# Kernel tuning notes

Hardware: AMD Instinct MI355X
Metric: run time of the kernel (lower is better)

The kernel has to match this reference:

```python
import jax, jax.numpy as jnp
import numpy as np

B, S, H = 8, 512, 1024          # batch, seq_len, hidden_size
T, K, FF = 8, 2, 4096           # num_thoughts, top_k, ffn dim (4*H)
NH = 8                          # combiner attention heads
HD = H // NH
CREATIVITY = 1.0


def setup_inputs() -> dict:
    key = jax.random.key(0)
    ks = jax.random.split(key, 16)
    s = 0.02
    return {
        "hidden_states": jax.random.normal(ks[0], (B, S, H), jnp.float32),
        # router
        "router_w": jax.random.normal(ks[1], (H, T), jnp.float32) * s,
        "router_b": jnp.zeros((T,), jnp.float32),
        # thought branch FFNs (one per thought)
        "W1": jax.random.normal(ks[2], (T, H, FF), jnp.float32) * s,
        "b1": jnp.zeros((T, FF), jnp.float32),
        "W2": jax.random.normal(ks[3], (T, FF, H), jnp.float32) * s,
        "b2": jnp.zeros((T, H), jnp.float32),
        # attention combiner (MultiheadAttention proj weights)
        "Wq": jax.random.normal(ks[4], (H, H), jnp.float32) * s,
        "bq": jnp.zeros((H,), jnp.float32),
        "Wk": jax.random.normal(ks[5], (H, H), jnp.float32) * s,
        "bk": jnp.zeros((H,), jnp.float32),
        "Wv": jax.random.normal(ks[6], (H, H), jnp.float32) * s,
        "bv": jnp.zeros((H,), jnp.float32),
        "Wo": jax.random.normal(ks[7], (H, H), jnp.float32) * s,
        "bo": jnp.zeros((H,), jnp.float32),
    }


def reference(hidden_states, router_w, router_b, W1, b1, W2, b2,
              Wq, bq, Wk, bk, Wv, bv, Wo, bo):
    # ---- router: mean-pool -> linear -> softmax -> top-k ----
    pooled = hidden_states.mean(axis=1)                       # [B,H]
    router_probs = jax.nn.softmax(pooled @ router_w + router_b, axis=-1)  # [B,T]
    top_p, top_i = jax.lax.top_k(router_probs, K)             # [B,K]
    weights = jax.nn.softmax(top_p, axis=-1)                  # renormalized active weights [B,K]

    # ---- grouped branch FFN (gather expert weights, batched GEMMs) ----
    h = jnp.einsum('bsh,bkhf->bksf', hidden_states, W1[top_i]) + b1[top_i][:, :, None, :]
    h = jax.nn.gelu(h, approximate=False)
    branch_out = jnp.einsum('bksf,bkfh->bksh', h, W2[top_i]) + b2[top_i][:, :, None, :]
    branch_out = branch_out * CREATIVITY                      # [B,K,S,H]

    # ---- attention combiner over flattened thoughts [B, K*S, H] ----
    L = K * S
    flat = branch_out.reshape(B, L, H)
    q = (flat @ Wq + bq).reshape(B, L, NH, HD)
    k = (flat @ Wk + bk).reshape(B, L, NH, HD)
    v = (flat @ Wv + bv).reshape(B, L, NH, HD)
    scores = jnp.einsum('blhd,bmhd->bhlm', q, k) / jnp.sqrt(jnp.float32(HD))
    attn = jax.nn.softmax(scores, axis=-1)
    ctx = jnp.einsum('bhlm,bmhd->blhd', attn, v).reshape(B, L, H)
    attended = (ctx @ Wo + bo).reshape(B, K, S, H)

    combined = jnp.einsum('bksh,bk->bsh', attended, weights)  # [B,S,H]

    # ---- metrics ----
    entropy = jnp.mean(-jnp.sum(router_probs * jnp.log(router_probs + 1e-8), axis=1))
    a = branch_out[:, 0].reshape(B, -1)
    b_ = branch_out[:, 1].reshape(B, -1)
    cos = jnp.sum(a * b_, -1) / jnp.maximum(
        jnp.linalg.norm(a, axis=-1) * jnp.linalg.norm(b_, axis=-1), 1e-8)
    diversity = jnp.mean(1.0 - cos)
    return combined, entropy, diversity
```

## Files before the change

### kernel.cpp

```cpp
#include <hip/hip_runtime.h>
#include <hip/hip_bf16.h>
#include <math.h>

typedef float f32x4 __attribute__((ext_vector_type(4)));
typedef short s16x8 __attribute__((ext_vector_type(8)));
typedef short s16x4 __attribute__((ext_vector_type(4)));
typedef unsigned int u32;

#define DEVI __device__ __forceinline__

#define Bn   8
#define Sn   512
#define Hn   1024
#define Tn   8
#define Kn   2
#define FFn  4096
#define NHn  8
#define HDn  128
#define Ln   1024
#define OUT_COMBINED 4194304

DEVI unsigned short f2bf(float x) {
  __hip_bfloat16 h = __float2bfloat16(x);
  union { __hip_bfloat16 h; unsigned short u; } cv; cv.h = h; return cv.u;
}
DEVI float bf2f(unsigned short u) {
  union { u32 i; float f; } cv; cv.i = ((u32)u) << 16; return cv.f;
}

typedef __attribute__((address_space(3))) u32 lds_u32;
typedef __attribute__((address_space(1))) u32 glb_u32;
DEVI void gload16(const void* g, void* l) {
  __builtin_amdgcn_global_load_lds((const glb_u32*)g, (lds_u32*)l, 16, 0, 0);
}

__global__ __launch_bounds__(256) void pool_part_k(const float* __restrict__ hid, float* __restrict__ part)
{
  const int b = blockIdx.x, scn = blockIdx.y;
  const int hh = threadIdx.x * 4;
  float4 acc = make_float4(0.f, 0.f, 0.f, 0.f);
  const float* base = hid + ((long)b * Sn + (long)scn * 128) * Hn + hh;
  for (int s = 0; s < 128; ++s) {
    float4 v = *(const float4*)(base + (long)s * Hn);
    acc.x += v.x; acc.y += v.y; acc.z += v.z; acc.w += v.w;
  }
  *(float4*)(part + ((long)(scn * Bn + b)) * Hn + hh) = acc;
}

__global__ __launch_bounds__(256) void pool_final_k(const float* __restrict__ part, float* __restrict__ pooled)
{
  const int i = blockIdx.x * 256 + threadIdx.x;
  float s = 0.f;
  for (int sc = 0; sc < 4; ++sc) s += part[sc * (Bn * Hn) + i];
  pooled[i] = s * (1.f / (float)Sn);
}

__global__ __launch_bounds__(64) void router_k(
    const float* __restrict__ pooled, const float* __restrict__ rw, const float* __restrict__ rb,
    float* __restrict__ probs, int* __restrict__ topi, float* __restrict__ wts,
    int* __restrict__ flags, float* __restrict__ entropy_out)
{
  __shared__ float lg[64];
  __shared__ int sfl[8];
  __shared__ float sent[8];
  const int tid = threadIdx.x;
  const int b = tid >> 3, t = tid & 7;
  if (tid < 8) sfl[tid] = 0;
  float acc = rb[t];
  const float* pb = pooled + b * Hn;
  for (int i = 0; i < Hn; ++i) acc += pb[i] * rw[i * Tn + t];
  lg[tid] = acc;
  __syncthreads();
  if (t == 0) {
    float p[8];
    float mx = lg[b * 8];
    for (int i = 1; i < 8; ++i) mx = fmaxf(mx, lg[b * 8 + i]);
    float ssum = 0.f;
    for (int i = 0; i < 8; ++i) { p[i] = expf(lg[b * 8 + i] - mx); ssum += p[i]; }
    float ent = 0.f;
    for (int i = 0; i < 8; ++i) { p[i] /= ssum; ent -= p[i] * logf(p[i] + 1e-8f); probs[b * 8 + i] = p[i]; }
    sent[b] = ent;
    int i1 = 0;
    for (int i = 1; i < 8; ++i) if (p[i] > p[i1]) i1 = i;
    int i2 = (i1 == 0) ? 1 : 0;
    for (int i = 0; i < 8; ++i) if (i != i1 && p[i] > p[i2]) i2 = i;
    float w0 = 1.f / (1.f + expf(p[i2] - p[i1]));
    float w1 = 1.f / (1.f + expf(p[i1] - p[i2]));
    topi[b * 2] = i1; topi[b * 2 + 1] = i2;
    wts[b * 2] = w0; wts[b * 2 + 1] = w1;
    atomicOr(&sfl[i1], 1); atomicOr(&sfl[i2], 1);
  }
  __syncthreads();
  if (tid < 8) flags[tid] = sfl[tid];
  if (tid == 0) {
    float e = 0.f;
    for (int i = 0; i < 8; ++i) e += sent[i];
    entropy_out[0] = e * (1.f / (float)Bn);
  }
}

__global__ __launch_bounds__(256) void cvt_k(const float* __restrict__ in, unsigned short* __restrict__ out)
{
  const long i = ((long)blockIdx.x * 256 + threadIdx.x) * 4;
  float4 v = *(const float4*)(in + i);
  s16x4 o;
  o[0] = (short)f2bf(v.x); o[1] = (short)f2bf(v.y); o[2] = (short)f2bf(v.z); o[3] = (short)f2bf(v.w);
  *(s16x4*)(out + i) = o;
}

__global__ __launch_bounds__(256) void bias3_k(const float* __restrict__ bq, const float* __restrict__ bk,
                                               const float* __restrict__ bv, float* __restrict__ o)
{
  const int i = blockIdx.x * 256 + threadIdx.x;
  o[i] = bq[i]; o[i + 1024] = bk[i]; o[i + 2048] = bv[i];
}

__global__ __launch_bounds__(256) void transpose_k(const float* __restrict__ Win, unsigned short* __restrict__ Wout,
                                                   int Kd, int N, long sIn, long sOut, const int* __restrict__ flags)
{
  const int t = blockIdx.z;
  if (flags && flags[t] == 0) return;
  __shared__ float tile[64][65];
  const float* in = Win + (long)t * sIn;
  unsigned short* out = Wout + (long)t * sOut;
  const int kb = blockIdx.y * 64, nb = blockIdx.x * 64;
  const int tx = threadIdx.x & 15, ty = threadIdx.x >> 4;
  #pragma unroll
  for (int i = 0; i < 4; ++i) {
    const int r = ty + i * 16;
    float4 v = *(const float4*)(in + (long)(kb + r) * N + nb + tx * 4);
    tile[r][tx * 4 + 0] = v.x; tile[r][tx * 4 + 1] = v.y;
    tile[r][tx * 4 + 2] = v.z; tile[r][tx * 4 + 3] = v.w;
  }
  __syncthreads();
  #pragma unroll
  for (int i = 0; i < 4; ++i) {
    const int n = ty + i * 16;
    s16x4 o;
    #pragma unroll
    for (int j = 0; j < 4; ++j) o[j] = (short)f2bf(tile[tx * 4 + j][n]);
    *(s16x4*)(out + (long)(nb + n) * Kd + kb + tx * 4) = o;
  }
}

template<int EPI, int OUTMODE>
__global__ __launch_bounds__(256) void gemm_k(
    const unsigned short* __restrict__ A0, const unsigned short* __restrict__ Bt0,
    const float* __restrict__ bias0, unsigned short* __restrict__ C0,
    int N, int Kd,
    const int* __restrict__ topi, int kTop,
    long sA_b, long sA_p, long sBt_t, int sBias_t, long sC_p)
{
  __shared__ __align__(16) char smem[36864];
  const int z = blockIdx.z;
  const int bidx = kTop ? (z / kTop) : 0;
  const int t = topi ? topi[z] : 0;
  const unsigned short* A = A0 + (long)bidx * sA_b + (long)z * sA_p;
  const unsigned short* Bt = Bt0 + (long)t * sBt_t;
  const float* bias = bias0 + (long)t * sBias_t;
  unsigned short* C = C0 + (long)z * sC_p;

  const int m0 = blockIdx.y * 128;
  const int n0 = blockIdx.x * 128;
  const int tid = threadIdx.x;
  const int lane = tid & 63, w = tid >> 6;
  const int wm = w >> 1, wn = w & 1;

  const int srow = w * 32 + (lane >> 2);
  const int csw = ((lane & 3) ^ ((srow ^ (srow >> 2)) & 3)) << 4;

  const char* gA0 = (const char*)(A + (long)(m0 + srow) * Kd) + csw;
  const char* gA1 = (const char*)(A + (long)(m0 + srow + 16) * Kd) + csw;
  const char* gB0 = (const char*)(Bt + (long)(n0 + srow) * Kd) + csw;
  const char* gB1 = (const char*)(Bt + (long)(n0 + srow + 16) * Kd) + csw;

  char* ldsAw = smem + w * 2048;
  char* ldsBw = smem + 16384 + w * 2048;

  f32x4 acc[4][4];
  const f32x4 zero = {0.f, 0.f, 0.f, 0.f};
  #pragma unroll
  for (int i = 0; i < 4; ++i)
    #pragma unroll
    for (int j = 0; j < 4; ++j) acc[i][j] = zero;

  const int rA = lane & 15;
  const int cb = (lane >> 4) << 4;
  int aoff[4], boff[4];
  #pragma unroll
  for (int mi = 0; mi < 4; ++mi) {
    int row = wm * 64 + mi * 16 + rA;
    aoff[mi] = row * 64 + (cb ^ (((row ^ (row >> 2)) & 3) << 4));
    int rowb = wn * 64 + mi * 16 + rA;
    boff[mi] = rowb * 64 + (cb ^ (((rowb ^ (rowb >> 2)) & 3) << 4));
  }

  const int nIter = Kd >> 5;
  gload16(gA0, ldsAw);
  gload16(gA1, ldsAw + 1024);
  gload16(gB0, ldsBw);
  gload16(gB1, ldsBw + 1024);
  __syncthreads();

  int cur = 0;
  for (int it = 0; it < nIter; ++it) {
    if (it + 1 < nIter) {
      const long kb2 = (long)(it + 1) * 64;
      const int nb = cur ^ 1;
      gload16(gA0 + kb2, ldsAw + nb * 8192);
      gload16(gA1 + kb2, ldsAw + nb * 8192 + 1024);
      gload16(gB0 + kb2, ldsBw + nb * 8192);
      gload16(gB1 + kb2, ldsBw + nb * 8192 + 1024);
    }
    const char* pa = smem + cur * 8192;
    const char* pb = smem + 16384 + cur * 8192;
    s16x8 af[4], bfr[4];
    #pragma unroll
    for (int mi = 0; mi < 4; ++mi) af[mi] = *(const s16x8*)(pa + aoff[mi]);
    #pragma unroll
    for (int nj = 0; nj < 4; ++nj) bfr[nj] = *(const s16x8*)(pb + boff[nj]);
    __builtin_amdgcn_s_setprio(1);
    #pragma unroll
    for (int mi = 0; mi < 4; ++mi)
      #pragma unroll
      for (int nj = 0; nj < 4; ++nj)
        acc[mi][nj] = __builtin_amdgcn_mfma_f32_16x16x32_bf16(af[mi], bfr[nj], acc[mi][nj], 0, 0, 0);
    __builtin_amdgcn_s_setprio(0);
    __syncthreads();
    cur ^= 1;
  }

  unsigned short* et = (unsigned short*)(smem + w * 9216);
  const int r4 = (lane >> 4) << 2;
  const int nbase = n0 + wn * 64;
  const int seg = nbase >> 10;
  #pragma unroll
  for (int nj = 0; nj < 4; ++nj) {
    const int n = nbase + nj * 16 + rA;
    const float bv = bias[n];
    #pragma unroll
    for (int mi = 0; mi < 4; ++mi) {
      #pragma unroll
      for (int j = 0; j < 4; ++j) {
        float x = acc[mi][nj][j] + bv;
        if (EPI == 1) x = 0.5f * x * (1.0f + erff(x * 0.70710678118654752f));
        const int mrl = mi * 16 + r4 + j;
        const int ncl = nj * 16 + rA;
        if (OUTMODE == 0 || seg < 2) et[mrl * 72 + ncl] = f2bf(x);
        else                         et[ncl * 72 + mrl] = f2bf(x);
      }
    }
  }
  const int erow = lane >> 3, echunk = lane & 7;
  if (OUTMODE == 0) {
    const long r0 = m0 + wm * 64;
    #pragma unroll
    for (int rr = 0; rr < 8; ++rr) {
      const int row = rr * 8 + erow;
      s16x8 v = *(const s16x8*)(et + row * 72 + echunk * 8);
      *(s16x8*)(C + (r0 + row) * N + nbase + echunk * 8) = v;
    }
  } else {
    const int nseg = nbase & 1023;
    if (seg < 2) {
      unsigned short* dst = C + (long)seg * 8388608;
      const long r0 = m0 + wm * 64;
      #pragma unroll
      for (int rr = 0; rr < 8; ++rr) {
        const int row = rr * 8 + erow;
        s16x8 v = *(const s16x8*)(et + row * 72 + echunk * 8);
        *(s16x8*)(dst + (r0 + row) * 1024 + nseg + echunk * 8) = v;
      }
    } else {
      unsigned short* vtp = C + 16777216;
      const int bb = m0 >> 10;
      const int ltok0 = (m0 & 1023) + wm * 64;
      #pragma unroll
      for (int rr = 0; rr < 8; ++rr) {
        const int nrow = rr * 8 + erow;
        s16x8 v = *(const s16x8*)(et + nrow * 72 + echunk * 8);
        *(s16x8*)(vtp + ((long)(bb * 1024 + nseg + nrow)) * 1024 + ltok0 + echunk * 8) = v;
      }
    }
  }
}

__global__ __launch_bounds__(256) void flash_k(
    const unsigned short* __restrict__ q, const unsigned short* __restrict__ k,
    const unsigned short* __restrict__ vt, unsigned short* __restrict__ ctx)
{
  __shared__ unsigned short Ks[64 * 128];
  __shared__ unsigned short Vs[128 * 64];
  __shared__ unsigned short Ps[4][16 * 72];
  const int qt = blockIdx.x, h = blockIdx.y, b = blockIdx.z;
  const int tid = threadIdx.x, lane = tid & 63, w = tid >> 6;
  const int q0 = qt * 64;
  const int rA = lane & 15;

  const int qrow = q0 + w * 16 + rA;
  const unsigned short* qp = q + ((long)(b * Ln + qrow)) * Hn + h * HDn + ((lane >> 4) * 8);
  s16x8 qf[4];
  #pragma unroll
  for (int kk = 0; kk < 4; ++kk) qf[kk] = *(const s16x8*)(qp + kk * 32);

  f32x4 o[8];
  const f32x4 zero = {0.f, 0.f, 0.f, 0.f};
  #pragma unroll
  for (int i = 0; i < 8; ++i) o[i] = zero;
  float mrun[4], lrun[4];
  #pragma unroll
  for (int j = 0; j < 4; ++j) { mrun[j] = -1e30f; lrun[j] = 0.f; }

  const float sc = 0.08838834764831845f * 1.4426950408889634f;

  const int krow0 = w * 16 + (lane >> 4);
  const int kc = lane & 15;
  const int vrow0 = w * 32 + (lane >> 3);
  const int vc = lane & 7;

  for (int kvt = 0; kvt < 16; ++kvt) {
    const int kv0 = kvt * 64;
    __syncthreads();
    #pragma unroll
    for (int qq = 0; qq < 4; ++qq) {
      const int rk = krow0 + qq * 4;
      gload16(k + ((long)(b * Ln + kv0 + rk)) * Hn + h * HDn + ((kc ^ (rk & 7)) * 8),
              (char*)Ks + w * 4096 + qq * 1024);
      const int rv = vrow0 + qq * 8;
      gload16(vt + ((long)(b * 1024 + h * HDn + rv)) * Ln + kv0 + ((vc ^ (rv & 7)) * 8),
              (char*)Vs + w * 4096 + qq * 1024);
    }
    __syncthreads();

    f32x4 sacc[4];
    #pragma unroll
    for (int nj = 0; nj < 4; ++nj) sacc[nj] = zero;
    #pragma unroll
    for (int kk = 0; kk < 4; ++kk) {
      #pragma unroll
      for (int nj = 0; nj < 4; ++nj) {
        const int row = nj * 16 + rA;
        const int byt = row * 256 + (((kk * 4 + (lane >> 4)) ^ (row & 7)) << 4);
        s16x8 kf = *(const s16x8*)((const char*)Ks + byt);
        sacc[nj] = __builtin_amdgcn_mfma_f32_16x16x32_bf16(qf[kk], kf, sacc[nj], 0, 0, 0);
      }
    }

    #pragma unroll
    for (int j = 0; j < 4; ++j) {
      float s0 = sacc[0][j] * sc, s1 = sacc[1][j] * sc, s2 = sacc[2][j] * sc, s3 = sacc[3][j] * sc;
      float tmax = fmaxf(fmaxf(s0, s1), fmaxf(s2, s3));
      #pragma unroll
      for (int mm = 1; mm < 16; mm <<= 1) tmax = fmaxf(tmax, __shfl_xor(tmax, mm, 64));
      const float mn = fmaxf(mrun[j], tmax);
      const float al = exp2f(mrun[j] - mn);
      mrun[j] = mn;
      float p0 = exp2f(s0 - mn), p1 = exp2f(s1 - mn), p2 = exp2f(s2 - mn), p3 = exp2f(s3 - mn);
      float ts = p0 + p1 + p2 + p3;
      #pragma unroll
      for (int mm = 1; mm < 16; mm <<= 1) ts += __shfl_xor(ts, mm, 64);
      lrun[j] = lrun[j] * al + ts;
      #pragma unroll
      for (int nn = 0; nn < 8; ++nn) o[nn][j] *= al;
      const int prow = ((lane >> 4) * 4 + j) * 72;
      Ps[w][prow + 0 * 16 + rA] = f2bf(p0);
      Ps[w][prow + 1 * 16 + rA] = f2bf(p1);
      Ps[w][prow + 2 * 16 + rA] = f2bf(p2);
      Ps[w][prow + 3 * 16 + rA] = f2bf(p3);
    }

    s16x8 pf[2];
    #pragma unroll
    for (int kk2 = 0; kk2 < 2; ++kk2)
      pf[kk2] = *(const s16x8*)((const char*)&Ps[w][0] + rA * 144 + kk2 * 64 + ((lane >> 4) << 4));
    #pragma unroll
    for (int kk2 = 0; kk2 < 2; ++kk2) {
      #pragma unroll
      for (int nn = 0; nn < 8; ++nn) {
        const int row = nn * 16 + rA;
        const int byt = row * 128 + (((kk2 * 4 + (lane >> 4)) ^ (row & 7)) << 4);
        s16x8 vf = *(const s16x8*)((const char*)Vs + byt);
        o[nn] = __builtin_amdgcn_mfma_f32_16x16x32_bf16(pf[kk2], vf, o[nn], 0, 0, 0);
      }
    }
  }

  #pragma unroll
  for (int nn = 0; nn < 8; ++nn) {
    #pragma unroll
    for (int j = 0; j < 4; ++j) {
      const int row = q0 + w * 16 + ((lane >> 4) << 2) + j;
      ctx[((long)(b * Ln + row)) * Hn + h * HDn + nn * 16 + rA] = f2bf(o[nn][j] / lrun[j]);
    }
  }
}

__global__ __launch_bounds__(256) void div_part_k(const unsigned short* __restrict__ br, float* __restrict__ part)
{
  const int b = blockIdx.y, ch = blockIdx.x;
  const unsigned short* a = br + (long)b * (2L * Sn * Hn);
  const unsigned short* c = a + (long)Sn * Hn;
  const int base = ch * 16384 + threadIdx.x * 8;
  float dot = 0.f, na = 0.f, nb = 0.f;
  #pragma unroll
  for (int i = 0; i < 8; ++i) {
    const int idx = base + i * 2048;
    s16x8 av = *(const s16x8*)(a + idx);
    s16x8 cv = *(const s16x8*)(c + idx);
    #pragma unroll
    for (int e = 0; e < 8; ++e) {
      float fa = bf2f((unsigned short)av[e]);
      float fc = bf2f((unsigned short)cv[e]);
      dot += fa * fc; na += fa * fa; nb += fc * fc;
    }
  }
  #pragma unroll
  for (int mm = 1; mm < 64; mm <<= 1) {
    dot += __shfl_xor(dot, mm, 64);
    na  += __shfl_xor(na, mm, 64);
    nb  += __shfl_xor(nb, mm, 64);
  }
  __shared__ float red[12];
  const int lane = threadIdx.x & 63, w = threadIdx.x >> 6;
  if (lane == 0) { red[w * 3] = dot; red[w * 3 + 1] = na; red[w * 3 + 2] = nb; }
  __syncthreads();
  if (threadIdx.x == 0) {
    float d = 0, x = 0, y = 0;
    for (int i = 0; i < 4; ++i) { d += red[i * 3]; x += red[i * 3 + 1]; y += red[i * 3 + 2]; }
    float* op = part + ((long)(b * 32 + ch)) * 3;
    op[0] = d; op[1] = x; op[2] = y;
  }
}

__global__ __launch_bounds__(64) void div_final_k(const float* __restrict__ part, float* __restrict__ outp)
{
  __shared__ float cosr[8];
  const int tid = threadIdx.x;
  if (tid < 8) {
    float d = 0, x = 0, y = 0;
    for (int i = 0; i < 32; ++i) {
      const float* p = part + ((long)(tid * 32 + i)) * 3;
      d += p[0]; x += p[1]; y += p[2];
    }
    cosr[tid] = d / fmaxf(sqrtf(x) * sqrtf(y), 1e-8f);
  }
  __syncthreads();
  if (tid == 0) {
    float s = 0.f;
    for (int i = 0; i < 8; ++i) s += 1.f - cosr[i];
    outp[0] = s * (1.f / 8.f);
  }
}

__global__ __launch_bounds__(256) void combine_k(const unsigned short* __restrict__ att,
                                                 const float* __restrict__ wts, float* __restrict__ out)
{
  const long i = ((long)blockIdx.x * 256 + threadIdx.x) * 8;
  const int b = (int)(i >> 19);
  const long rem = i & 524287;
  const unsigned short* a0 = att + (long)b * (2L * Sn * Hn) + rem;
  const unsigned short* a1 = a0 + (long)Sn * Hn;
  const float w0 = wts[b * 2], w1 = wts[b * 2 + 1];
  s16x8 v0 = *(const s16x8*)a0;
  s16x8 v1 = *(const s16x8*)a1;
  float r[8];
  #pragma unroll
  for (int e = 0; e < 8; ++e) r[e] = w0 * bf2f((unsigned short)v0[e]) + w1 * bf2f((unsigned short)v1[e]);
  *(float4*)(out + i)     = make_float4(r[0], r[1], r[2], r[3]);
  *(float4*)(out + i + 4) = make_float4(r[4], r[5], r[6], r[7]);
}

extern "C" void kernel_launch(void* const* d_in, const int* in_sizes, int n_in,
                              void* d_out, int out_size, void* d_ws, size_t ws_size,
                              hipStream_t stream)
{
  (void)in_sizes; (void)n_in; (void)out_size; (void)ws_size;
  const float* hidden   = (const float*)d_in[0];
  const float* router_w = (const float*)d_in[1];
  const float* router_b = (const float*)d_in[2];
  const float* W1 = (const float*)d_in[3];
  const float* b1 = (const float*)d_in[4];
  const float* W2 = (const float*)d_in[5];
  const float* b2 = (const float*)d_in[6];
  const float* Wq = (const float*)d_in[7];
  const float* bq = (const float*)d_in[8];
  const float* Wk = (const float*)d_in[9];
  const float* bk = (const float*)d_in[10];
  const float* Wv = (const float*)d_in[11];
  const float* bv = (const float*)d_in[12];
  const float* Wo = (const float*)d_in[13];
  const float* bo = (const float*)d_in[14];
  float* out = (float*)d_out;

  char* ws = (char*)d_ws;
  float* pooled  = (float*)(ws);
  float* ppart   = (float*)(ws + 32768);
  float* probs   = (float*)(ws + 163840);
  int*   topi    = (int*)  (ws + 164096);
  float* wts     = (float*)(ws + 164352);
  int*   flags   = (int*)  (ws + 164608);
  float* dpart   = (float*)(ws + 164864);
  float* qkvbias = (float*)(ws + 167936);
  unsigned short* hid_bf = (unsigned short*)(ws + 262144);
  unsigned short* Wt     = (unsigned short*)(ws + 262144 + 8388608);
  unsigned short* hbuf   = (unsigned short*)(ws + 262144 + 8388608 + 67108864);
  unsigned short* br     = (unsigned short*)(ws + 262144 + 8388608 + 134217728);
  unsigned short* wqkvo  = (unsigned short*)(ws + 262144 + 8388608 + 134217728 + 16777216);
  unsigned short* qb  = Wt;
  unsigned short* kbf = Wt + 8388608;
  unsigned short* vt  = Wt + 16777216;
  unsigned short* ctx = hbuf;
  unsigned short* att = hbuf + 8388608;
  unsigned short* wqt = wqkvo;
  unsigned short* wkt = wqkvo + 1048576;
  unsigned short* wvt = wqkvo + 2097152;
  unsigned short* wot = wqkvo + 3145728;

  pool_part_k<<<dim3(Bn, 4), 256, 0, stream>>>(hidden, ppart);
  pool_final_k<<<dim3(32), 256, 0, stream>>>(ppart, pooled);
  router_k<<<1, 64, 0, stream>>>(pooled, router_w, router_b, probs, topi, wts, flags, out + OUT_COMBINED);

  cvt_k<<<4096, 256, 0, stream>>>(hidden, hid_bf);
  bias3_k<<<4, 256, 0, stream>>>(bq, bk, bv, qkvbias);
  transpose_k<<<dim3(64, 16, Tn), 256, 0, stream>>>(W1, Wt, Hn, FFn, (long)Hn * FFn, (long)FFn * Hn, flags);
  transpose_k<<<dim3(16, 16, 1), 256, 0, stream>>>(Wq, wqt, Hn, Hn, 0, 0, nullptr);
  transpose_k<<<dim3(16, 16, 1), 256, 0, stream>>>(Wk, wkt, Hn, Hn, 0, 0, nullptr);
  transpose_k<<<dim3(16, 16, 1), 256, 0, stream>>>(Wv, wvt, Hn, Hn, 0, 0, nullptr);
  transpose_k<<<dim3(16, 16, 1), 256, 0, stream>>>(Wo, wot, Hn, Hn, 0, 0, nullptr);

  gemm_k<1, 0><<<dim3(FFn / 128, Sn / 128, 16), 256, 0, stream>>>(
      hid_bf, Wt, b1, hbuf, FFn, Hn, topi, 2,
      (long)Sn * Hn, 0L, (long)FFn * Hn, FFn, (long)Sn * FFn);

  transpose_k<<<dim3(16, 64, Tn), 256, 0, stream>>>(W2, Wt, FFn, Hn, (long)FFn * Hn, (long)Hn * FFn, flags);

  gemm_k<0, 0><<<dim3(Hn / 128, Sn / 128, 16), 256, 0, stream>>>(
      hbuf, Wt, b2, br, Hn, FFn, topi, 2,
      0L, (long)Sn * FFn, (long)Hn * FFn, Hn, (long)Sn * Hn);

  div_part_k<<<dim3(32, Bn), 256, 0, stream>>>(br, dpart);
  div_final_k<<<1, 64, 0, stream>>>(dpart, out + OUT_COMBINED + 1);

  gemm_k<0, 1><<<dim3(3072 / 128, (Bn * Ln) / 128, 1), 256, 0, stream>>>(
      br, wqkvo, qkvbias, qb, 3072, Hn, nullptr, 0, 0L, 0L, 0L, 0, 0L);

  flash_k<<<dim3(Ln / 64, NHn, Bn), 256, 0, stream>>>(qb, kbf, vt, ctx);

  gemm_k<0, 0><<<dim3(Hn / 128, (Bn * Ln) / 128, 1), 256, 0, stream>>>(
      ctx, wot, bo, att, Hn, Hn, nullptr, 0, 0L, 0L, 0L, 0, 0L);

  combine_k<<<2048, 256, 0, stream>>>(att, wts, out);
}
```

Before: 558.8 us.

## Process 32 query rows per wave in flash attention with lazy max rescaling

Each wave in the flash attention kernel now handles two 16-row query tiles (128 queries per block), so every K and V fragment read from LDS feeds two MFMAs and the grid shrinks by half. The per-row online softmax is replaced by a single wave-wide running max that is only updated and rescaled when some score exceeds it by more than 8 (in log2 units). The row sum is now reduced across lanes once at the end rather than every tile. This cuts LDS traffic, shuffles and rescaling work, at the cost of more registers and fewer blocks (512), which may reduce occupancy. The shared-max trick also risks precision loss if scores within a wave differ widely.

```diff
diff --git a/kernel.cpp b/kernel.cpp
--- a/kernel.cpp
+++ b/kernel.cpp
@@ -291,29 +291,36 @@
 {
   __shared__ unsigned short Ks[64 * 128];
   __shared__ unsigned short Vs[128 * 64];
-  __shared__ unsigned short Ps[4][16 * 72];
+  __shared__ unsigned short Ps[4][32 * 72];
   const int qt = blockIdx.x, h = blockIdx.y, b = blockIdx.z;
   const int tid = threadIdx.x, lane = tid & 63, w = tid >> 6;
-  const int q0 = qt * 64;
-  const int rA = lane & 15;
-
-  const int qrow = q0 + w * 16 + rA;
-  const unsigned short* qp = q + ((long)(b * Ln + qrow)) * Hn + h * HDn + ((lane >> 4) * 8);
-  s16x8 qf[4];
-  #pragma unroll
-  for (int kk = 0; kk < 4; ++kk) qf[kk] = *(const s16x8*)(qp + kk * 32);
-
-  f32x4 o[8];
+  const int rA = lane & 15, g = lane >> 4;
+  const int q0w = qt * 128 + w * 32;
+
+  s16x8 qf[2][4];
+  #pragma unroll
+  for (int qi = 0; qi < 2; ++qi) {
+    const unsigned short* qp = q + ((long)(b * Ln + q0w + qi * 16 + rA)) * Hn + h * HDn + g * 8;
+    #pragma unroll
+    for (int kk = 0; kk < 4; ++kk) qf[qi][kk] = *(const s16x8*)(qp + kk * 32);
+  }
+
+  f32x4 o[2][8];
   const f32x4 zero = {0.f, 0.f, 0.f, 0.f};
   #pragma unroll
-  for (int i = 0; i < 8; ++i) o[i] = zero;
-  float mrun[4], lrun[4];
-  #pragma unroll
-  for (int j = 0; j < 4; ++j) { mrun[j] = -1e30f; lrun[j] = 0.f; }
-
-  const float sc = 0.08838834764831845f * 1.4426950408889634f;
-
-  const int krow0 = w * 16 + (lane >> 4);
+  for (int qi = 0; qi < 2; ++qi)
+    #pragma unroll
+    for (int nn = 0; nn < 8; ++nn) o[qi][nn] = zero;
+  float lrun[2][4];
+  #pragma unroll
+  for (int qi = 0; qi < 2; ++qi)
+    #pragma unroll
+    for (int j = 0; j < 4; ++j) lrun[qi][j] = 0.f;
+  float m = 0.f;
+
+  const float sc2 = 0.08838834764831845f * 1.4426950408889634f;
+
+  const int krow0 = w * 16 + g;
   const int kc = lane & 15;
   const int vrow0 = w * 32 + (lane >> 3);
   const int vc = lane & 7;
@@ -332,67 +339,104 @@
     }
     __syncthreads();
 
-    f32x4 sacc[4];
-    #pragma unroll
-    for (int nj = 0; nj < 4; ++nj) sacc[nj] = zero;
+    f32x4 sacc[2][4];
+    #pragma unroll
+    for (int qi = 0; qi < 2; ++qi)
+      #pragma unroll
+      for (int nj = 0; nj < 4; ++nj) sacc[qi][nj] = zero;
     #pragma unroll
     for (int kk = 0; kk < 4; ++kk) {
       #pragma unroll
       for (int nj = 0; nj < 4; ++nj) {
         const int row = nj * 16 + rA;
-        const int byt = row * 256 + (((kk * 4 + (lane >> 4)) ^ (row & 7)) << 4);
+        const int byt = row * 256 + (((kk * 4 + g) ^ (row & 7)) << 4);
         s16x8 kf = *(const s16x8*)((const char*)Ks + byt);
-        sacc[nj] = __builtin_amdgcn_mfma_f32_16x16x32_bf16(qf[kk], kf, sacc[nj], 0, 0, 0);
-      }
-    }
-
-    #pragma unroll
-    for (int j = 0; j < 4; ++j) {
-      float s0 = sacc[0][j] * sc, s1 = sacc[1][j] * sc, s2 = sacc[2][j] * sc, s3 = sacc[3][j] * sc;
-      float tmax = fmaxf(fmaxf(s0, s1), fmaxf(s2, s3));
-      #pragma unroll
-      for (int mm = 1; mm < 16; mm <<= 1) tmax = fmaxf(tmax, __shfl_xor(tmax, mm, 64));
-      const float mn = fmaxf(mrun[j], tmax);
-      const float al = exp2f(mrun[j] - mn);
-      mrun[j] = mn;
-      float p0 = exp2f(s0 - mn), p1 = exp2f(s1 - mn), p2 = exp2f(s2 - mn), p3 = exp2f(s3 - mn);
-      float ts = p0 + p1 + p2 + p3;
-      #pragma unroll
-      for (int mm = 1; mm < 16; mm <<= 1) ts += __shfl_xor(ts, mm, 64);
-      lrun[j] = lrun[j] * al + ts;
-      #pragma unroll
-      for (int nn = 0; nn < 8; ++nn) o[nn][j] *= al;
-      const int prow = ((lane >> 4) * 4 + j) * 72;
-      Ps[w][prow + 0 * 16 + rA] = f2bf(p0);
-      Ps[w][prow + 1 * 16 + rA] = f2bf(p1);
-      Ps[w][prow + 2 * 16 + rA] = f2bf(p2);
-      Ps[w][prow + 3 * 16 + rA] = f2bf(p3);
-    }
-
-    s16x8 pf[2];
-    #pragma unroll
-    for (int kk2 = 0; kk2 < 2; ++kk2)
-      pf[kk2] = *(const s16x8*)((const char*)&Ps[w][0] + rA * 144 + kk2 * 64 + ((lane >> 4) << 4));
+        sacc[0][nj] = __builtin_amdgcn_mfma_f32_16x16x32_bf16(qf[0][kk], kf, sacc[0][nj], 0, 0, 0);
+        sacc[1][nj] = __builtin_amdgcn_mfma_f32_16x16x32_bf16(qf[1][kk], kf, sacc[1][nj], 0, 0, 0);
+      }
+    }
+
+    float vmax = -3.0e38f;
+    #pragma unroll
+    for (int qi = 0; qi < 2; ++qi)
+      #pragma unroll
+      for (int nj = 0; nj < 4; ++nj)
+        #pragma unroll
+        for (int j = 0; j < 4; ++j) {
+          const float s = sacc[qi][nj][j] * sc2;
+          sacc[qi][nj][j] = s;
+          vmax = fmaxf(vmax, s);
+        }
+    if (!__all(vmax <= m + 8.0f)) {
+      float mn = vmax;
+      #pragma unroll
+      for (int mm = 1; mm < 64; mm <<= 1) mn = fmaxf(mn, __shfl_xor(mn, mm, 64));
+      const float al = exp2f(m - mn);
+      #pragma unroll
+      for (int qi = 0; qi < 2; ++qi) {
+        #pragma unroll
+        for (int nn = 0; nn < 8; ++nn)
+          #pragma unroll
+          for (int j = 0; j < 4; ++j) o[qi][nn][j] *= al;
+        #pragma unroll
+        for (int j = 0; j < 4; ++j) lrun[qi][j] *= al;
+      }
+      m = mn;
+    }
+    #pragma unroll
+    for (int qi = 0; qi < 2; ++qi)
+      #pragma unroll
+      for (int j = 0; j < 4; ++j) {
+        float p0 = exp2f(sacc[qi][0][j] - m);
+        float p1 = exp2f(sacc[qi][1][j] - m);
+        float p2 = exp2f(sacc[qi][2][j] - m);
+        float p3 = exp2f(sacc[qi][3][j] - m);
+        lrun[qi][j] += (p0 + p1) + (p2 + p3);
+        const int prow = (qi * 16 + g * 4 + j) * 72;
+        Ps[w][prow + 0 * 16 + rA] = f2bf(p0);
+        Ps[w][prow + 1 * 16 + rA] = f2bf(p1);
+        Ps[w][prow + 2 * 16 + rA] = f2bf(p2);
+        Ps[w][prow + 3 * 16 + rA] = f2bf(p3);
+      }
+
+    s16x8 pf[2][2];
+    #pragma unroll
+    for (int qi = 0; qi < 2; ++qi)
+      #pragma unroll
+      for (int kk2 = 0; kk2 < 2; ++kk2)
+        pf[qi][kk2] = *(const s16x8*)(&Ps[w][(qi * 16 + rA) * 72 + kk2 * 32 + g * 8]);
     #pragma unroll
     for (int kk2 = 0; kk2 < 2; ++kk2) {
       #pragma unroll
       for (int nn = 0; nn < 8; ++nn) {
         const int row = nn * 16 + rA;
-        const int byt = row * 128 + (((kk2 * 4 + (lane >> 4)) ^ (row & 7)) << 4);
+        const int byt = row * 128 + (((kk2 * 4 + g) ^ (row & 7)) << 4);
         s16x8 vf = *(const s16x8*)((const char*)Vs + byt);
-        o[nn] = __builtin_amdgcn_mfma_f32_16x16x32_bf16(pf[kk2], vf, o[nn], 0, 0, 0);
-      }
-    }
-  }
-
-  #pragma unroll
-  for (int nn = 0; nn < 8; ++nn) {
+        o[0][nn] = __builtin_amdgcn_mfma_f32_16x16x32_bf16(pf[0][kk2], vf, o[0][nn], 0, 0, 0);
+        o[1][nn] = __builtin_amdgcn_mfma_f32_16x16x32_bf16(pf[1][kk2], vf, o[1][nn], 0, 0, 0);
+      }
+    }
+  }
+
+  float linv[2][4];
+  #pragma unroll
+  for (int qi = 0; qi < 2; ++qi)
     #pragma unroll
     for (int j = 0; j < 4; ++j) {
-      const int row = q0 + w * 16 + ((lane >> 4) << 2) + j;
-      ctx[((long)(b * Ln + row)) * Hn + h * HDn + nn * 16 + rA] = f2bf(o[nn][j] / lrun[j]);
-    }
-  }
+      float l = lrun[qi][j];
+      #pragma unroll
+      for (int mm = 1; mm < 16; mm <<= 1) l += __shfl_xor(l, mm, 64);
+      linv[qi][j] = 1.0f / l;
+    }
+  #pragma unroll
+  for (int qi = 0; qi < 2; ++qi)
+    #pragma unroll
+    for (int nn = 0; nn < 8; ++nn)
+      #pragma unroll
+      for (int j = 0; j < 4; ++j) {
+        const int row = q0w + qi * 16 + g * 4 + j;
+        ctx[((long)(b * Ln + row)) * Hn + h * HDn + nn * 16 + rA] = f2bf(o[qi][nn][j] * linv[qi][j]);
+      }
 }
 
 __global__ __launch_bounds__(256) void div_part_k(const unsigned short* __restrict__ br, float* __restrict__ part)
@@ -544,7 +588,7 @@
   gemm_k<0, 1><<<dim3(3072 / 128, (Bn * Ln) / 128, 1), 256, 0, stream>>>(
       br, wqkvo, qkvbias, qb, 3072, Hn, nullptr, 0, 0L, 0L, 0L, 0, 0L);
 
-  flash_k<<<dim3(Ln / 64, NHn, Bn), 256, 0, stream>>>(qb, kbf, vt, ctx);
+  flash_k<<<dim3(Ln / 128, NHn, Bn), 256, 0, stream>>>(qb, kbf, vt, ctx);
 
   gemm_k<0, 0><<<dim3(Hn / 128, (Bn * Ln) / 128, 1), 256, 0, stream>>>(
       ctx, wot, bo, att, Hn, Hn, nullptr, 0, 0L, 0L, 0L, 0, 0L);
```

After: 538.0 us. 1.04x faster.
